# Optimization experiments

Hardware: AMD Instinct MI355X
Metric: run time of the kernel (lower is better)

## Reference

```python
import jax, jax.numpy as jnp
import numpy as np

B, T, F, H = 8192, 256, 64, 50

def setup_inputs() -> dict:
    key = jax.random.key(0)
    ks = jax.random.split(key, 6)
    s = 0.1
    x = jax.random.normal(ks[0], (B, T, F), dtype=jnp.float32)
    W = jax.random.normal(ks[1], (F, 3 * H), dtype=jnp.float32) * s   # input kernel [z|r|h]
    U = jax.random.normal(ks[2], (H, 3 * H), dtype=jnp.float32) * s   # recurrent kernel
    b = jax.random.normal(ks[3], (2, 3 * H), dtype=jnp.float32) * s   # [input bias; recurrent bias] (reset_after=True)
    Wd = jax.random.normal(ks[4], (H, 1), dtype=jnp.float32) * s
    bd = jax.random.normal(ks[5], (1,), dtype=jnp.float32) * s
    return {"x": x, "W": W, "U": U, "b": b, "Wd": Wd, "bd": bd}

def _gru_last_hidden(x, W, U, b):
    # Precompute input projections for all timesteps: [B,T,3H]
    xp = jnp.einsum('btf,fg->btg', x, W) + b[0]
    xp = jnp.transpose(xp, (1, 0, 2))  # [T,B,3H] for scan over time
    bi = b[1]

    def step(h, xt):
        rp = h @ U + bi                       # recurrent projection [B,3H]
        xz, xr, xh = jnp.split(xt, 3, axis=-1)
        rz, rr, rh = jnp.split(rp, 3, axis=-1)
        z = jax.nn.sigmoid(xz + rz)
        r = jax.nn.sigmoid(xr + rr)
        hh = jnp.tanh(xh + r * rh)            # reset_after=True formulation
        h_new = z * h + (1.0 - z) * hh
        return h_new, None

    h0 = jnp.zeros((x.shape[0], U.shape[0]), dtype=x.dtype)
    h_last, _ = jax.lax.scan(step, h0, xp)
    return h_last

def reference(x, W, U, b, Wd, bd):
    h = _gru_last_hidden(x, W, U, b)   # [B,H]
    # Dropout is identity at inference time
    return h @ Wd + bd                 # [B,1]
```

## Files before the change

kernel.cpp:

```cpp
#include <hip/hip_runtime.h>
#include <hip/hip_bf16.h>


typedef __attribute__((ext_vector_type(8))) short s16x8;
typedef __attribute__((ext_vector_type(4))) short s16x4;
typedef __attribute__((ext_vector_type(4))) float f32x4;

#define TS 256

__device__ __forceinline__ unsigned short f2bf(float f) {
  return __builtin_bit_cast(unsigned short, __float2bfloat16(f));
}

__global__ __launch_bounds__(256, 2) void gru_fused(
    const float* __restrict__ x,  const float* __restrict__ W,
    const float* __restrict__ U,  const float* __restrict__ b,
    const float* __restrict__ Wd, const float* __restrict__ bdp,
    float* __restrict__ out)
{
  __shared__ __align__(16) unsigned short xbuf[2][2][512];
  __shared__ __align__(16) unsigned short hbuf[2][2][512];
  __shared__ float red[4][16];

  const int tid = threadIdx.x;
  const int l   = tid & 63;
  const int w   = tid >> 6;
  const int lhi = l >> 4, llo = l & 15;
  const int row0 = blockIdx.x << 4;
  const int u = (w << 4) + llo;

  ((unsigned long long*)hbuf)[tid]       = 0ULL;
  ((unsigned long long*)hbuf)[tid + 256] = 0ULL;

  float bz = 0.f, br = 0.f, bh0 = 0.f, bh1 = 0.f;
  if (u < 50) {
    bz  = b[u]       + b[150 + u];
    br  = b[50 + u]  + b[200 + u];
    bh0 = b[100 + u];
    bh1 = b[250 + u];
  }

  s16x8 breg[3][4];
  #pragma unroll
  for (int g = 0; g < 3; ++g) {
    #pragma unroll
    for (int kc = 0; kc < 4; ++kc) {
      s16x8 f;
      #pragma unroll
      for (int i = 0; i < 8; ++i) {
        const int k = kc * 32 + lhi * 8 + i;
        float v = 0.f;
        if (u < 50 && k < 114)
          v = (k < 64) ? W[k * 150 + g * 50 + u]
                       : U[(k - 64) * 150 + g * 50 + u];
        f[i] = (short)f2bf(v);
      }
      breg[g][kc] = f;
    }
  }

  const int sc    = tid >> 7;
  const int sla   = (tid >> 1) & 63;
  const int shalf = tid & 1;
  const float* xp = x + (long)(row0 + (sla & 15)) * (TS * 64)
                      + sc * 32 + (sla >> 4) * 8 + shalf * 4;
  unsigned short* const xdst0 = &xbuf[0][sc][sla * 8 + shalf * 4];
  unsigned short* const xdst1 = &xbuf[1][sc][sla * 8 + shalf * 4];

  f32x4 xc = *(const f32x4*)xp;
  {
    s16x4 pk;
    pk[0] = (short)f2bf(xc[0]); pk[1] = (short)f2bf(xc[1]);
    pk[2] = (short)f2bf(xc[2]); pk[3] = (short)f2bf(xc[3]);
    *(s16x4*)xdst0 = pk;
  }
  xc = *(const f32x4*)(xp + 64);
  __syncthreads();

  float h0 = 0.f, h1 = 0.f, h2 = 0.f, h3 = 0.f;
  f32x4 xn;

#define GRU_STEP(T, XC, XN, PR, PW, XDST)                                      \
  {                                                                            \
    int tpre = (T) + 2; if (tpre > TS - 1) tpre = TS - 1;                      \
    XN = *(const f32x4*)(xp + (long)tpre * 64);                                \
    const s16x8 a0 = *(const s16x8*)&xbuf[PR][0][l * 8];                       \
    const s16x8 a1 = *(const s16x8*)&xbuf[PR][1][l * 8];                       \
    const s16x8 a2 = *(const s16x8*)&hbuf[PR][0][l * 8];                       \
    const s16x8 a3 = *(const s16x8*)&hbuf[PR][1][l * 8];                       \
    f32x4 lo[3], hi[3];                                                        \
    _Pragma("unroll")                                                          \
    for (int g = 0; g < 3; ++g) {                                              \
      f32x4 zz = {0.f, 0.f, 0.f, 0.f};                                         \
      zz    = __builtin_amdgcn_mfma_f32_16x16x32_bf16(a2, breg[g][2], zz, 0,0,0);\
      hi[g] = __builtin_amdgcn_mfma_f32_16x16x32_bf16(a3, breg[g][3], zz, 0,0,0);\
      f32x4 yy = {0.f, 0.f, 0.f, 0.f};                                         \
      yy    = __builtin_amdgcn_mfma_f32_16x16x32_bf16(a0, breg[g][0], yy, 0,0,0);\
      lo[g] = __builtin_amdgcn_mfma_f32_16x16x32_bf16(a1, breg[g][1], yy, 0,0,0);\
    }                                                                          \
    {                                                                          \
      s16x4 pk;                                                                \
      pk[0] = (short)f2bf(XC[0]); pk[1] = (short)f2bf(XC[1]);                  \
      pk[2] = (short)f2bf(XC[2]); pk[3] = (short)f2bf(XC[3]);                  \
      *(s16x4*)(XDST) = pk;                                                    \
    }                                                                          \
    _Pragma("unroll")                                                          \
    for (int r = 0; r < 4; ++r) {                                              \
      float hv = (r == 0) ? h0 : (r == 1) ? h1 : (r == 2) ? h2 : h3;           \
      const float zs = lo[0][r] + hi[0][r] + bz;                               \
      const float rs = lo[1][r] + hi[1][r] + br;                               \
      const float z  = __builtin_amdgcn_rcpf(1.f + __expf(-zs));               \
      const float rr = __builtin_amdgcn_rcpf(1.f + __expf(-rs));               \
      const float ar = lo[2][r] + bh0 + rr * (hi[2][r] + bh1);                 \
      const float e  = __expf(2.f * ar);                                       \
      const float hh = 1.f - 2.f * __builtin_amdgcn_rcpf(1.f + e);             \
      hv = hh + z * (hv - hh);                                                 \
      if (r == 0) h0 = hv; else if (r == 1) h1 = hv;                           \
      else if (r == 2) h2 = hv; else h3 = hv;                                  \
      hbuf[PW][u >> 5][(((u & 31) >> 3) * 16 + lhi * 4 + r) * 8 + (u & 7)] =   \
          f2bf(hv);                                                            \
    }                                                                          \
    __syncthreads();                                                           \
  }

  for (int t = 0; t < TS; t += 2) {
    GRU_STEP(t,     xc, xn, 0, 1, xdst1)
    GRU_STEP(t + 1, xn, xc, 1, 0, xdst0)
  }
#undef GRU_STEP

  const float Wdv = (u < 50) ? Wd[u] : 0.f;
  float p0 = h0 * Wdv, p1 = h1 * Wdv, p2 = h2 * Wdv, p3 = h3 * Wdv;
  #pragma unroll
  for (int m = 1; m < 16; m <<= 1) {
    p0 += __shfl_xor(p0, m);
    p1 += __shfl_xor(p1, m);
    p2 += __shfl_xor(p2, m);
    p3 += __shfl_xor(p3, m);
  }
  if (llo == 0) {
    red[w][lhi * 4 + 0] = p0;
    red[w][lhi * 4 + 1] = p1;
    red[w][lhi * 4 + 2] = p2;
    red[w][lhi * 4 + 3] = p3;
  }
  __syncthreads();
  if (tid < 16)
    out[row0 + tid] =
        red[0][tid] + red[1][tid] + red[2][tid] + red[3][tid] + bdp[0];
}

extern "C" void kernel_launch(void* const* d_in, const int* in_sizes, int n_in,
                              void* d_out, int out_size, void* d_ws, size_t ws_size,
                              hipStream_t stream) {
  const float* x   = (const float*)d_in[0];
  const float* W   = (const float*)d_in[1];
  const float* U   = (const float*)d_in[2];
  const float* b   = (const float*)d_in[3];
  const float* Wd  = (const float*)d_in[4];
  const float* bdp = (const float*)d_in[5];
  float* out = (float*)d_out;
  gru_fused<<<dim3(512), dim3(256), 0, stream>>>(x, W, U, b, Wd, bdp, out);
}
```

Baseline: 827.5 us.

## Deepen x prefetch to four steps and use raw LDS-only barriers

Global loads of x are now issued four timesteps ahead, using eight rotating register buffers and an eight-step unrolled loop, where before they ran two steps ahead. This gives more time to hide global memory latency inside the serial recurrence. __syncthreads is replaced by a barrier that waits only on LDS counters (lgkmcnt), so outstanding global loads no longer stall each step's barrier. The cost is more registers per thread, which could hurt occupancy at 2 blocks per CU, and a larger unrolled code body.

```diff
diff --git a/kernel.cpp b/kernel.cpp
--- a/kernel.cpp
+++ b/kernel.cpp
@@ -11,6 +11,13 @@
 __device__ __forceinline__ unsigned short f2bf(float f) {
   return __builtin_bit_cast(unsigned short, __float2bfloat16(f));
 }
+
+#define RAWBAR()                                                \
+  do {                                                          \
+    asm volatile("s_waitcnt lgkmcnt(0)" ::: "memory");          \
+    __builtin_amdgcn_sched_barrier(0);                          \
+    __builtin_amdgcn_s_barrier();                               \
+  } while (0)
 
 __global__ __launch_bounds__(256, 2) void gru_fused(
     const float* __restrict__ x,  const float* __restrict__ W,
@@ -67,23 +74,26 @@
   unsigned short* const xdst0 = &xbuf[0][sc][sla * 8 + shalf * 4];
   unsigned short* const xdst1 = &xbuf[1][sc][sla * 8 + shalf * 4];
 
-  f32x4 xc = *(const f32x4*)xp;
   {
+    const f32x4 x0 = *(const f32x4*)xp;
     s16x4 pk;
-    pk[0] = (short)f2bf(xc[0]); pk[1] = (short)f2bf(xc[1]);
-    pk[2] = (short)f2bf(xc[2]); pk[3] = (short)f2bf(xc[3]);
+    pk[0] = (short)f2bf(x0[0]); pk[1] = (short)f2bf(x0[1]);
+    pk[2] = (short)f2bf(x0[2]); pk[3] = (short)f2bf(x0[3]);
     *(s16x4*)xdst0 = pk;
   }
-  xc = *(const f32x4*)(xp + 64);
-  __syncthreads();
+  f32x4 xA0 = *(const f32x4*)(xp + 1 * 64);
+  f32x4 xA1 = *(const f32x4*)(xp + 2 * 64);
+  f32x4 xA2 = *(const f32x4*)(xp + 3 * 64);
+  f32x4 xA3 = *(const f32x4*)(xp + 4 * 64);
+  f32x4 xB0, xB1, xB2, xB3;
+  RAWBAR();
 
   float h0 = 0.f, h1 = 0.f, h2 = 0.f, h3 = 0.f;
-  f32x4 xn;
 
-#define GRU_STEP(T, XC, XN, PR, PW, XDST)                                      \
+#define GRU_STEP(T, CUR, NXT, PR, XDST)                                        \
   {                                                                            \
-    int tpre = (T) + 2; if (tpre > TS - 1) tpre = TS - 1;                      \
-    XN = *(const f32x4*)(xp + (long)tpre * 64);                                \
+    const int tl = ((T) + 5 > TS - 1) ? (TS - 1) : ((T) + 5);                  \
+    NXT = *(const f32x4*)(xp + (long)tl * 64);                                 \
     const s16x8 a0 = *(const s16x8*)&xbuf[PR][0][l * 8];                       \
     const s16x8 a1 = *(const s16x8*)&xbuf[PR][1][l * 8];                       \
     const s16x8 a2 = *(const s16x8*)&hbuf[PR][0][l * 8];                       \
@@ -100,8 +110,8 @@
     }                                                                          \
     {                                                                          \
       s16x4 pk;                                                                \
-      pk[0] = (short)f2bf(XC[0]); pk[1] = (short)f2bf(XC[1]);                  \
-      pk[2] = (short)f2bf(XC[2]); pk[3] = (short)f2bf(XC[3]);                  \
+      pk[0] = (short)f2bf(CUR[0]); pk[1] = (short)f2bf(CUR[1]);                \
+      pk[2] = (short)f2bf(CUR[2]); pk[3] = (short)f2bf(CUR[3]);                \
       *(s16x4*)(XDST) = pk;                                                    \
     }                                                                          \
     _Pragma("unroll")                                                          \
@@ -117,15 +127,21 @@
       hv = hh + z * (hv - hh);                                                 \
       if (r == 0) h0 = hv; else if (r == 1) h1 = hv;                           \
       else if (r == 2) h2 = hv; else h3 = hv;                                  \
-      hbuf[PW][u >> 5][(((u & 31) >> 3) * 16 + lhi * 4 + r) * 8 + (u & 7)] =   \
-          f2bf(hv);                                                            \
+      hbuf[(PR) ^ 1][u >> 5]                                                   \
+          [(((u & 31) >> 3) * 16 + lhi * 4 + r) * 8 + (u & 7)] = f2bf(hv);     \
     }                                                                          \
-    __syncthreads();                                                           \
+    RAWBAR();                                                                  \
   }
 
-  for (int t = 0; t < TS; t += 2) {
-    GRU_STEP(t,     xc, xn, 0, 1, xdst1)
-    GRU_STEP(t + 1, xn, xc, 1, 0, xdst0)
+  for (int t = 0; t < TS; t += 8) {
+    GRU_STEP(t + 0, xA0, xB0, 0, xdst1)
+    GRU_STEP(t + 1, xA1, xB1, 1, xdst0)
+    GRU_STEP(t + 2, xA2, xB2, 0, xdst1)
+    GRU_STEP(t + 3, xA3, xB3, 1, xdst0)
+    GRU_STEP(t + 4, xB0, xA0, 0, xdst1)
+    GRU_STEP(t + 5, xB1, xA1, 1, xdst0)
+    GRU_STEP(t + 6, xB2, xA2, 0, xdst1)
+    GRU_STEP(t + 7, xB3, xA3, 1, xdst0)
   }
 #undef GRU_STEP
 
```

New measurement: 783.7 us. -5.3%, faster.

## Software-pipeline input projection one step ahead and prescale gates for exp2

Applied to the files above, without the earlier changes.

Computes the input-projection MFMAs for step t+1 during step t so that only the recurrent MFMAs sit on the serial critical path. Folds the log2(e) scaling into the weights and biases so the activations use exp2 directly. Deepens the global x prefetch to 4 steps, switches to packed bf16 conversion via inline asm, and replaces __syncthreads with a raw lgkmcnt wait plus s_barrier. This adds register pressure from more live prefetch buffers and accumulators, and relies on hand-written barrier semantics being correct.

```diff
diff --git a/kernel.cpp b/kernel.cpp
--- a/kernel.cpp
+++ b/kernel.cpp
@@ -3,14 +3,30 @@
 
 
 typedef __attribute__((ext_vector_type(8))) short s16x8;
-typedef __attribute__((ext_vector_type(4))) short s16x4;
 typedef __attribute__((ext_vector_type(4))) float f32x4;
 
 #define TS 256
 
 __device__ __forceinline__ unsigned short f2bf(float f) {
-  return __builtin_bit_cast(unsigned short, __float2bfloat16(f));
-}
+  unsigned int v = __builtin_bit_cast(unsigned int, f);
+  v += 0x7FFFu + ((v >> 16) & 1u);
+  return (unsigned short)(v >> 16);
+}
+__device__ __forceinline__ unsigned int cvtpk(float a, float b) {
+  unsigned int r;
+  asm("v_cvt_pk_bf16_f32 %0, %1, %2" : "=v"(r) : "v"(a), "v"(b));
+  return r;
+}
+__device__ __forceinline__ float rcpf(float a) {
+  return __builtin_amdgcn_rcpf(a);
+}
+
+#define RAWBAR()                                                \
+  do {                                                          \
+    asm volatile("s_waitcnt lgkmcnt(0)" ::: "memory");          \
+    __builtin_amdgcn_sched_barrier(0);                          \
+    __builtin_amdgcn_s_barrier();                               \
+  } while (0)
 
 __global__ __launch_bounds__(256, 2) void gru_fused(
     const float* __restrict__ x,  const float* __restrict__ W,
@@ -29,20 +45,22 @@
   const int row0 = blockIdx.x << 4;
   const int u = (w << 4) + llo;
 
-  ((unsigned long long*)hbuf)[tid]       = 0ULL;
-  ((unsigned long long*)hbuf)[tid + 256] = 0ULL;
-
-  float bz = 0.f, br = 0.f, bh0 = 0.f, bh1 = 0.f;
+  ((unsigned long long*)hbuf)[tid] = 0ULL;
+
+  const float sZR = -1.44269504088896f;
+  const float sH  =  2.88539008177793f;
+  float bzS = 0.f, brS = 0.f, bh0S = 0.f, bh1S = 0.f;
   if (u < 50) {
-    bz  = b[u]       + b[150 + u];
-    br  = b[50 + u]  + b[200 + u];
-    bh0 = b[100 + u];
-    bh1 = b[250 + u];
+    bzS  = sZR * (b[u]      + b[150 + u]);
+    brS  = sZR * (b[50 + u] + b[200 + u]);
+    bh0S = sH * b[100 + u];
+    bh1S = sH * b[250 + u];
   }
 
   s16x8 breg[3][4];
   #pragma unroll
   for (int g = 0; g < 3; ++g) {
+    const float sc = (g < 2) ? sZR : sH;
     #pragma unroll
     for (int kc = 0; kc < 4; ++kc) {
       s16x8 f;
@@ -53,7 +71,7 @@
         if (u < 50 && k < 114)
           v = (k < 64) ? W[k * 150 + g * 50 + u]
                        : U[(k - 64) * 150 + g * 50 + u];
-        f[i] = (short)f2bf(v);
+        f[i] = (short)f2bf(v * sc);
       }
       breg[g][kc] = f;
     }
@@ -64,70 +82,97 @@
   const int shalf = tid & 1;
   const float* xp = x + (long)(row0 + (sla & 15)) * (TS * 64)
                       + sc * 32 + (sla >> 4) * 8 + shalf * 4;
-  unsigned short* const xdst0 = &xbuf[0][sc][sla * 8 + shalf * 4];
-  unsigned short* const xdst1 = &xbuf[1][sc][sla * 8 + shalf * 4];
-
-  f32x4 xc = *(const f32x4*)xp;
+  unsigned long long* const xd0 =
+      (unsigned long long*)&xbuf[0][sc][sla * 8 + shalf * 4];
+  unsigned long long* const xd1 =
+      (unsigned long long*)&xbuf[1][sc][sla * 8 + shalf * 4];
+
+  unsigned short* const hst =
+      &hbuf[0][u >> 5][(((u & 31) >> 3) * 16 + lhi * 4) * 8 + (u & 7)];
+
   {
-    s16x4 pk;
-    pk[0] = (short)f2bf(xc[0]); pk[1] = (short)f2bf(xc[1]);
-    pk[2] = (short)f2bf(xc[2]); pk[3] = (short)f2bf(xc[3]);
-    *(s16x4*)xdst0 = pk;
-  }
-  xc = *(const f32x4*)(xp + 64);
+    const f32x4 t0 = *(const f32x4*)xp;
+    *xd0 = ((unsigned long long)cvtpk(t0[2], t0[3]) << 32) | cvtpk(t0[0], t0[1]);
+    const f32x4 t1 = *(const f32x4*)(xp + 64);
+    *xd1 = ((unsigned long long)cvtpk(t1[2], t1[3]) << 32) | cvtpk(t1[0], t1[1]);
+  }
+  f32x4 X0, X1, X2, X3, X4, X5, X6, X7;
+  X2 = *(const f32x4*)(xp + 2 * 64);
+  X3 = *(const f32x4*)(xp + 3 * 64);
+  X4 = *(const f32x4*)(xp + 4 * 64);
+  X5 = *(const f32x4*)(xp + 5 * 64);
   __syncthreads();
 
+  f32x4 LA0 = {bzS, bzS, bzS, bzS}, LA1 = {brS, brS, brS, brS},
+        LA2 = {bh0S, bh0S, bh0S, bh0S}, LB0, LB1, LB2;
+  {
+    const s16x8 a0 = *(const s16x8*)&xbuf[0][0][l * 8];
+    const s16x8 a1 = *(const s16x8*)&xbuf[0][1][l * 8];
+    LA0 = __builtin_amdgcn_mfma_f32_16x16x32_bf16(a0, breg[0][0], LA0, 0,0,0);
+    LA0 = __builtin_amdgcn_mfma_f32_16x16x32_bf16(a1, breg[0][1], LA0, 0,0,0);
+    LA1 = __builtin_amdgcn_mfma_f32_16x16x32_bf16(a0, breg[1][0], LA1, 0,0,0);
+    LA1 = __builtin_amdgcn_mfma_f32_16x16x32_bf16(a1, breg[1][1], LA1, 0,0,0);
+    LA2 = __builtin_amdgcn_mfma_f32_16x16x32_bf16(a0, breg[2][0], LA2, 0,0,0);
+    LA2 = __builtin_amdgcn_mfma_f32_16x16x32_bf16(a1, breg[2][1], LA2, 0,0,0);
+  }
+  __syncthreads();
+
   float h0 = 0.f, h1 = 0.f, h2 = 0.f, h3 = 0.f;
-  f32x4 xn;
-
-#define GRU_STEP(T, XC, XN, PR, PW, XDST)                                      \
+
+#define STEP(T, XC, XL, C0, C1, C2, N0, N1, N2)                                \
   {                                                                            \
-    int tpre = (T) + 2; if (tpre > TS - 1) tpre = TS - 1;                      \
-    XN = *(const f32x4*)(xp + (long)tpre * 64);                                \
-    const s16x8 a0 = *(const s16x8*)&xbuf[PR][0][l * 8];                       \
-    const s16x8 a1 = *(const s16x8*)&xbuf[PR][1][l * 8];                       \
-    const s16x8 a2 = *(const s16x8*)&hbuf[PR][0][l * 8];                       \
-    const s16x8 a3 = *(const s16x8*)&hbuf[PR][1][l * 8];                       \
-    f32x4 lo[3], hi[3];                                                        \
-    _Pragma("unroll")                                                          \
-    for (int g = 0; g < 3; ++g) {                                              \
-      f32x4 zz = {0.f, 0.f, 0.f, 0.f};                                         \
-      zz    = __builtin_amdgcn_mfma_f32_16x16x32_bf16(a2, breg[g][2], zz, 0,0,0);\
-      hi[g] = __builtin_amdgcn_mfma_f32_16x16x32_bf16(a3, breg[g][3], zz, 0,0,0);\
-      f32x4 yy = {0.f, 0.f, 0.f, 0.f};                                         \
-      yy    = __builtin_amdgcn_mfma_f32_16x16x32_bf16(a0, breg[g][0], yy, 0,0,0);\
-      lo[g] = __builtin_amdgcn_mfma_f32_16x16x32_bf16(a1, breg[g][1], yy, 0,0,0);\
-    }                                                                          \
-    {                                                                          \
-      s16x4 pk;                                                                \
-      pk[0] = (short)f2bf(XC[0]); pk[1] = (short)f2bf(XC[1]);                  \
-      pk[2] = (short)f2bf(XC[2]); pk[3] = (short)f2bf(XC[3]);                  \
-      *(s16x4*)(XDST) = pk;                                                    \
-    }                                                                          \
+    const int tl = ((T) + 6 > TS - 1) ? (TS - 1) : ((T) + 6);                  \
+    XL = *(const f32x4*)(xp + (long)tl * 64);                                  \
+    const int PAR = (T) & 1;                                                   \
+    const s16x8 a2 = *(const s16x8*)&hbuf[PAR][0][l * 8];                      \
+    const s16x8 a3 = *(const s16x8*)&hbuf[PAR][1][l * 8];                      \
+    f32x4 g0 = {0.f, 0.f, 0.f, 0.f}, g1 = {0.f, 0.f, 0.f, 0.f};               \
+    f32x4 g2 = {bh1S, bh1S, bh1S, bh1S};                                       \
+    g0 = __builtin_amdgcn_mfma_f32_16x16x32_bf16(a2, breg[0][2], g0, 0,0,0);   \
+    g0 = __builtin_amdgcn_mfma_f32_16x16x32_bf16(a3, breg[0][3], g0, 0,0,0);   \
+    g1 = __builtin_amdgcn_mfma_f32_16x16x32_bf16(a2, breg[1][2], g1, 0,0,0);   \
+    g1 = __builtin_amdgcn_mfma_f32_16x16x32_bf16(a3, breg[1][3], g1, 0,0,0);   \
+    g2 = __builtin_amdgcn_mfma_f32_16x16x32_bf16(a2, breg[2][2], g2, 0,0,0);   \
+    g2 = __builtin_amdgcn_mfma_f32_16x16x32_bf16(a3, breg[2][3], g2, 0,0,0);   \
+    const s16x8 a0 = *(const s16x8*)&xbuf[PAR ^ 1][0][l * 8];                  \
+    const s16x8 a1 = *(const s16x8*)&xbuf[PAR ^ 1][1][l * 8];                  \
+    N0 = (f32x4){bzS, bzS, bzS, bzS};                                          \
+    N1 = (f32x4){brS, brS, brS, brS};                                          \
+    N2 = (f32x4){bh0S, bh0S, bh0S, bh0S};                                      \
+    N0 = __builtin_amdgcn_mfma_f32_16x16x32_bf16(a0, breg[0][0], N0, 0,0,0);   \
+    N0 = __builtin_amdgcn_mfma_f32_16x16x32_bf16(a1, breg[0][1], N0, 0,0,0);   \
+    N1 = __builtin_amdgcn_mfma_f32_16x16x32_bf16(a0, breg[1][0], N1, 0,0,0);   \
+    N1 = __builtin_amdgcn_mfma_f32_16x16x32_bf16(a1, breg[1][1], N1, 0,0,0);   \
+    N2 = __builtin_amdgcn_mfma_f32_16x16x32_bf16(a0, breg[2][0], N2, 0,0,0);   \
+    N2 = __builtin_amdgcn_mfma_f32_16x16x32_bf16(a1, breg[2][1], N2, 0,0,0);   \
+    *(PAR ? xd1 : xd0) =                                                       \
+        ((unsigned long long)cvtpk(XC[2], XC[3]) << 32) | cvtpk(XC[0], XC[1]); \
     _Pragma("unroll")                                                          \
     for (int r = 0; r < 4; ++r) {                                              \
       float hv = (r == 0) ? h0 : (r == 1) ? h1 : (r == 2) ? h2 : h3;           \
-      const float zs = lo[0][r] + hi[0][r] + bz;                               \
-      const float rs = lo[1][r] + hi[1][r] + br;                               \
-      const float z  = __builtin_amdgcn_rcpf(1.f + __expf(-zs));               \
-      const float rr = __builtin_amdgcn_rcpf(1.f + __expf(-rs));               \
-      const float ar = lo[2][r] + bh0 + rr * (hi[2][r] + bh1);                 \
-      const float e  = __expf(2.f * ar);                                       \
-      const float hh = 1.f - 2.f * __builtin_amdgcn_rcpf(1.f + e);             \
-      hv = hh + z * (hv - hh);                                                 \
+      const float z  = rcpf(1.f + exp2f(C0[r] + g0[r]));                       \
+      const float rr = rcpf(1.f + exp2f(C1[r] + g1[r]));                       \
+      const float q  = rcpf(1.f + exp2f(fmaf(rr, g2[r], C2[r])));              \
+      const float hh = fmaf(-2.f, q, 1.f);                                     \
+      hv = fmaf(z, hv - hh, hh);                                               \
       if (r == 0) h0 = hv; else if (r == 1) h1 = hv;                           \
       else if (r == 2) h2 = hv; else h3 = hv;                                  \
-      hbuf[PW][u >> 5][(((u & 31) >> 3) * 16 + lhi * 4 + r) * 8 + (u & 7)] =   \
-          f2bf(hv);                                                            \
+      hst[(PAR ^ 1) * 1024 + r * 8] = (unsigned short)cvtpk(hv, 0.f);          \
     }                                                                          \
-    __syncthreads();                                                           \
-  }
-
-  for (int t = 0; t < TS; t += 2) {
-    GRU_STEP(t,     xc, xn, 0, 1, xdst1)
-    GRU_STEP(t + 1, xn, xc, 1, 0, xdst0)
-  }
-#undef GRU_STEP
+    RAWBAR();                                                                  \
+  }
+
+  for (int t = 0; t < TS; t += 8) {
+    STEP(t + 0, X2, X6, LA0, LA1, LA2, LB0, LB1, LB2)
+    STEP(t + 1, X3, X7, LB0, LB1, LB2, LA0, LA1, LA2)
+    STEP(t + 2, X4, X0, LA0, LA1, LA2, LB0, LB1, LB2)
+    STEP(t + 3, X5, X1, LB0, LB1, LB2, LA0, LA1, LA2)
+    STEP(t + 4, X6, X2, LA0, LA1, LA2, LB0, LB1, LB2)
+    STEP(t + 5, X7, X3, LB0, LB1, LB2, LA0, LA1, LA2)
+    STEP(t + 6, X0, X4, LA0, LA1, LA2, LB0, LB1, LB2)
+    STEP(t + 7, X1, X5, LB0, LB1, LB2, LA0, LA1, LA2)
+  }
+#undef STEP
 
   const float Wdv = (u < 50) ? Wd[u] : 0.f;
   float p0 = h0 * Wdv, p1 = h1 * Wdv, p2 = h2 * Wdv, p3 = h3 * Wdv;
```

Result: faster. 798.1 us (-3.6%).
